# Performance work log

Measured on AMD Instinct MI355X. Metric: run time of the kernel, lower is better.

Reference implementation:

```python
import jax, jax.numpy as jnp
import numpy as np

HID = 1024   # hidden_size
NH = 16      # num_heads
NKV = 4      # num_kv_heads
HD = 64      # head_dim
C = 64       # chunk_size
RATIO = 0.125  # freq_cutoff_ratio
KS = 7       # conv_kernel_size


def setup_inputs() -> dict:
    key = jax.random.key(0)
    ks = jax.random.split(key, 11)
    B, N = 4, 4096
    s = 0.02
    return {
        "hidden_states": jax.random.normal(ks[0], (B, N, HID), jnp.float32),
        "q_w": jax.random.normal(ks[1], (NH * HD, HID), jnp.float32) * s,
        "k_w": jax.random.normal(ks[2], (NKV * HD, HID), jnp.float32) * s,
        "v_w": jax.random.normal(ks[3], (NKV * HD, HID), jnp.float32) * s,
        "o_w": jax.random.normal(ks[4], (HID, NH * HD), jnp.float32) * s,
        "dw_r": jax.random.normal(ks[5], (HID, 1, KS), jnp.float32) * 0.3,
        "pw_r": jax.random.normal(ks[6], (HID, HID), jnp.float32) * s,
        "dw_i": jax.random.normal(ks[7], (HID, 1, KS), jnp.float32) * 0.3,
        "pw_i": jax.random.normal(ks[8], (HID, HID), jnp.float32) * s,
        "gate_w": jax.random.normal(ks[9], (HID, HID), jnp.float32) * s,
        "alpha_raw": jnp.zeros((1,), jnp.float32),
    }


def _block_causal_attention(x, qw, kw, vw, ow, k):
    # x: [B, nc, k, D] real. Flatten chunk freq bins; chunk j attends to chunks 0..j.
    B, nc, _, D = x.shape
    T = nc * k
    xf = x.reshape(B, T, D)
    q = (xf @ qw.T).reshape(B, T, NH, HD).transpose(0, 2, 1, 3)    # [B,H,T,hd]
    kk = (xf @ kw.T).reshape(B, T, NKV, HD).transpose(0, 2, 1, 3)
    v = (xf @ vw.T).reshape(B, T, NKV, HD).transpose(0, 2, 1, 3)
    rep = NH // NKV
    kk = jnp.repeat(kk, rep, axis=1)
    v = jnp.repeat(v, rep, axis=1)
    chunk_ids = jnp.arange(T) // k
    mask = chunk_ids[:, None] >= chunk_ids[None, :]                # [T,T] bool
    scores = jnp.einsum('bhqd,bhkd->bhqk', q, kk) / np.float32(np.sqrt(HD))
    scores = jnp.where(mask[None, None], scores, jnp.finfo(scores.dtype).min)
    p = jax.nn.softmax(scores, axis=-1)
    o = jnp.einsum('bhqk,bhkd->bhqd', p, v)
    o = o.transpose(0, 2, 1, 3).reshape(B, T, NH * HD)
    return (o @ ow.T).reshape(B, nc, k, D)


def _causal_conv(x, dw, pw):
    # x: [B, nc, L, D] real. Depthwise causal conv + GELU + pointwise conv.
    B, nc, L, D = x.shape
    xc = x.reshape(B * nc, L, D).transpose(0, 2, 1)                # [BN, D, L]
    xp = jnp.pad(xc, ((0, 0), (0, 0), (KS - 1, 0)))                # causal left pad
    y = jax.lax.conv_general_dilated(
        xp, dw, window_strides=(1,), padding='VALID',
        dimension_numbers=('NCH', 'OIH', 'NCH'), feature_group_count=D)
    y = jax.nn.gelu(y, approximate=False)
    y = jnp.einsum('ncl,oc->nol', y, pw)                           # 1x1 conv
    return y.transpose(0, 2, 1).reshape(B, nc, L, D)


def _forward(hidden_states, q_w, k_w, v_w, o_w, dw_r, pw_r, dw_i, pw_i, gate_w, alpha_raw):
    B, N, D = hidden_states.shape
    pad_len = (-N) % C
    x = jnp.pad(hidden_states, ((0, 0), (0, pad_len), (0, 0))) if pad_len else hidden_states
    nc = x.shape[1] // C
    chunks = x.reshape(B, nc, C, D)
    Xh = jnp.fft.rfft(chunks.astype(jnp.float32), axis=2)          # [B,nc,M,D] complex
    M = Xh.shape[2]
    k = max(1, int(M * RATIO))
    X_low, X_high = Xh[:, :, :k, :], Xh[:, :, k:, :]
    # low-freq: block-causal attention on real and imag parts separately
    A_r = _block_causal_attention(X_low.real, q_w, k_w, v_w, o_w, k)
    A_i = _block_causal_attention(X_low.imag, q_w, k_w, v_w, o_w, k)
    A_low = jax.lax.complex(A_r, A_i)
    # high-freq: causal conv branch, gated by per-chunk time-domain mean
    H_r = _causal_conv(X_high.real, dw_r, pw_r)
    H_i = _causal_conv(X_high.imag, dw_i, pw_i)
    g = jax.nn.sigmoid(chunks.mean(axis=2) @ gate_w.T)[:, :, None, :]  # [B,nc,1,D]
    A_high = jax.lax.complex(H_r * g, H_i * g) + X_high
    alpha = jax.nn.sigmoid(alpha_raw)                               # [1]
    A_low_fused = alpha * A_low + (1.0 - alpha) * X_low
    Y_hat = jnp.concatenate([A_low_fused, A_high], axis=2)
    Y = jnp.fft.irfft(Y_hat, n=C, axis=2)
    return Y.reshape(B, -1, D)[:, :N, :].astype(hidden_states.dtype)


def reference(hidden_states, q_w, k_w, v_w, o_w, dw_r, pw_r, dw_i, pw_i, gate_w, alpha_raw):
    return _forward(hidden_states, q_w, k_w, v_w, o_w, dw_r, pw_r, dw_i, pw_i, gate_w, alpha_raw)
```

## Files before the change

### kernel.cpp

```cpp
#include <hip/hip_runtime.h>
#include <math.h>


typedef __bf16 bf16_t;
typedef bf16_t bf16x8 __attribute__((ext_vector_type(8)));
typedef float f32x4 __attribute__((ext_vector_type(4)));

#define EP_NONE 0
#define EP_SIGMOID 1
#define EP_FUSELOW 2
#define EP_HIGH 3

__device__ __forceinline__ void gld_lds16(const bf16_t* g, bf16_t* l) {
  __builtin_amdgcn_global_load_lds(
      (const __attribute__((address_space(1))) unsigned int*)g,
      (__attribute__((address_space(3))) unsigned int*)l, 16, 0, 0);
}

__global__ __launch_bounds__(256) void dft_kernel(const float* __restrict__ X,
                                                  bf16_t* __restrict__ Xh,
                                                  bf16_t* __restrict__ XLr,
                                                  bf16_t* __restrict__ XLi,
                                                  bf16_t* __restrict__ gmean) {
  const int d = blockIdx.x * 256 + threadIdx.x;
  const long bc = blockIdx.y;
  const int b = (int)(bc >> 6), ch = (int)(bc & 63);
  const float* xp = X + (bc * 64) * 1024 + d;
  float x[64];
#pragma unroll
  for (int t = 0; t < 64; t++) x[t] = xp[(long)t * 1024];
#pragma unroll
  for (int t = 0; t < 32; t++) {
    float a = x[t], bb = x[t + 32];
    x[t] = a + bb;
    x[t + 32] = a - bb;
  }
  bf16_t* outp = Xh + bc * 66 * 1024 + d;
  const float W = -6.283185307179586f / 64.f;
  for (int f = 0; f <= 32; f += 2) {
    float sd, cd;
    __sincosf(W * f, &sd, &cd);
    float c = 1.f, s = 0.f, ar = 0.f, ai = 0.f;
#pragma unroll
    for (int t = 0; t < 32; t++) {
      ar = fmaf(x[t], c, ar);
      ai = fmaf(x[t], s, ai);
      float cn = c * cd - s * sd;
      s = s * cd + c * sd;
      c = cn;
    }
    outp[(long)f * 1024] = (bf16_t)ar;
    outp[(long)(33 + f) * 1024] = (bf16_t)ai;
    if (f < 4) {
      long xr = ((long)(b * 256 + ch * 4 + f)) * 1024 + d;
      XLr[xr] = (bf16_t)ar;
      XLi[xr] = (bf16_t)ai;
    }
    if (f == 0) gmean[bc * 1024 + d] = (bf16_t)(ar * (1.f / 64.f));
  }
  for (int f = 1; f <= 31; f += 2) {
    float sd, cd;
    __sincosf(W * f, &sd, &cd);
    float c = 1.f, s = 0.f, ar = 0.f, ai = 0.f;
#pragma unroll
    for (int t = 0; t < 32; t++) {
      ar = fmaf(x[32 + t], c, ar);
      ai = fmaf(x[32 + t], s, ai);
      float cn = c * cd - s * sd;
      s = s * cd + c * sd;
      c = cn;
    }
    outp[(long)f * 1024] = (bf16_t)ar;
    outp[(long)(33 + f) * 1024] = (bf16_t)ai;
    if (f < 4) {
      long xr = ((long)(b * 256 + ch * 4 + f)) * 1024 + d;
      XLr[xr] = (bf16_t)ar;
      XLi[xr] = (bf16_t)ai;
    }
  }
}

__global__ __launch_bounds__(256) void concat_w(const float* __restrict__ qw,
                                                const float* __restrict__ kw,
                                                const float* __restrict__ vw,
                                                bf16_t* __restrict__ W) {
  int i = blockIdx.x * 256 + threadIdx.x;
  float4 v;
  if (i < 262144) v = ((const float4*)qw)[i];
  else if (i < 327680) v = ((const float4*)kw)[i - 262144];
  else v = ((const float4*)vw)[i - 327680];
  bf16_t* o = W + (long)i * 4;
  o[0] = (bf16_t)v.x; o[1] = (bf16_t)v.y; o[2] = (bf16_t)v.z; o[3] = (bf16_t)v.w;
}

__global__ __launch_bounds__(256) void cvt4_bf16(const float* __restrict__ s0,
                                                 const float* __restrict__ s1,
                                                 const float* __restrict__ s2,
                                                 const float* __restrict__ s3,
                                                 bf16_t* __restrict__ d0,
                                                 bf16_t* __restrict__ d1,
                                                 bf16_t* __restrict__ d2,
                                                 bf16_t* __restrict__ d3) {
  int i = blockIdx.x * 256 + threadIdx.x;
  const float* s = blockIdx.y == 0 ? s0 : blockIdx.y == 1 ? s1 : blockIdx.y == 2 ? s2 : s3;
  bf16_t* dst = blockIdx.y == 0 ? d0 : blockIdx.y == 1 ? d1 : blockIdx.y == 2 ? d2 : d3;
  float4 v = ((const float4*)s)[i];
  bf16_t* o = dst + (long)i * 4;
  o[0] = (bf16_t)v.x; o[1] = (bf16_t)v.y; o[2] = (bf16_t)v.z; o[3] = (bf16_t)v.w;
}

__global__ __launch_bounds__(256) void mk_basis(bf16_t* __restrict__ bhi,
                                                bf16_t* __restrict__ bres,
                                                float* __restrict__ tlow) {
  int idx = blockIdx.x * 256 + threadIdx.x;
  const float TW = 6.283185307179586f / 64.f;
  if (idx < 4096) {
    int t = idx >> 6, k = idx & 63;
    float v = 0.f;
    if (k < 28) {
      int ft = ((4 + k) * t) & 63;
      v = 2.f * cosf(TW * (float)ft) * (1.f / 64.f);
    } else if (k == 28) {
      int ft = (32 * t) & 63;
      v = cosf(TW * (float)ft) * (1.f / 64.f);
    } else if (k < 57) {
      int ft = ((k - 25) * t) & 63;
      v = -2.f * sinf(TW * (float)ft) * (1.f / 64.f);
    }
    bf16_t h = (bf16_t)v;
    float res = v - (float)h;
    int addr = t * 64 + (((k >> 3) ^ (t & 7)) << 3) + (k & 7);
    bhi[addr] = h;
    bres[addr] = (bf16_t)res;
  } else if (idx < 4608) {
    int i = idx - 4096;
    int t = i >> 3, j = i & 7;
    float v = 0.f;
    if (j == 0) v = 1.f / 64.f;
    else if (j < 7) {
      int f = (j + 1) >> 1;
      int ft = (f * t) & 63;
      float th = TW * (float)ft;
      v = (j & 1) ? 2.f * cosf(th) * (1.f / 64.f)
                  : -2.f * sinf(th) * (1.f / 64.f);
    }
    tlow[i] = v;
  }
}

template <int EMODE>
__global__ __launch_bounds__(256) void mmbf_kernel(
    const bf16_t* __restrict__ A0, const bf16_t* __restrict__ A1,
    const bf16_t* __restrict__ B0, const bf16_t* __restrict__ B1,
    int N, int K,
    void* __restrict__ C0v, void* __restrict__ C1v,
    const bf16_t* __restrict__ E0, const bf16_t* __restrict__ E1,
    bf16_t* __restrict__ XhMut,
    const float* __restrict__ gate, const float* __restrict__ alpha_ptr) {
  constexpr int BM = 128, BN = 128, BK = 32;
  __shared__ bf16_t As[BM * BK];
  __shared__ bf16_t Bs[BN * BK];
  const int z = blockIdx.z;
  const bf16_t* A = z ? A1 : A0;
  const bf16_t* B = z ? B1 : B0;
  void* Cv = z ? C1v : C0v;
  const bf16_t* E = z ? E1 : E0;
  const int imoff = z ? 33 * 1024 : 0;
  const int tid = threadIdx.x;
  const int lane = tid & 63;
  const int wave = tid >> 6;
  const int wm = (wave & 1) * 64, wn = (wave >> 1) * 64;
  const int m0 = blockIdx.x * BM, n0 = blockIdx.y * BN;
  const int q = lane >> 4, mr = lane & 15;
  const int lrow = lane >> 2, lk8 = (lane & 3) * 8;

  f32x4 acc[4][4];
#pragma unroll
  for (int i = 0; i < 4; i++)
#pragma unroll
    for (int j = 0; j < 4; j++) acc[i][j] = (f32x4){0.f, 0.f, 0.f, 0.f};

  const long arow0 = (long)(m0 + wave * 16 + lrow) * K + lk8;
  const long brow0 = (long)(n0 + wave * 16 + lrow) * K + lk8;

  for (int kb = 0; kb < K; kb += BK) {
#pragma unroll
    for (int it = 0; it < 2; it++) {
      gld_lds16(A + arow0 + (long)it * 64 * K + kb, As + (wave * 16 + it * 64) * BK);
      gld_lds16(B + brow0 + (long)it * 64 * K + kb, Bs + (wave * 16 + it * 64) * BK);
    }
    __syncthreads();
    bf16x8 af[4], bfr[4];
#pragma unroll
    for (int mi = 0; mi < 4; mi++)
      af[mi] = *(const bf16x8*)&As[(wm + mi * 16 + mr) * BK + q * 8];
#pragma unroll
    for (int ni = 0; ni < 4; ni++)
      bfr[ni] = *(const bf16x8*)&Bs[(wn + ni * 16 + mr) * BK + q * 8];
#pragma unroll
    for (int mi = 0; mi < 4; mi++)
#pragma unroll
      for (int ni = 0; ni < 4; ni++)
        acc[mi][ni] = __builtin_amdgcn_mfma_f32_16x16x32_bf16(
            af[mi], bfr[ni], acc[mi][ni], 0, 0, 0);
    __syncthreads();
  }

  float alpha = 0.f;
  if constexpr (EMODE == EP_FUSELOW) alpha = 1.f / (1.f + __expf(-alpha_ptr[0]));
#pragma unroll
  for (int mi = 0; mi < 4; mi++) {
#pragma unroll
    for (int ni = 0; ni < 4; ni++) {
      int col = n0 + wn + ni * 16 + mr;
      int rbase = m0 + wm + mi * 16 + q * 4;
#pragma unroll
      for (int r = 0; r < 4; r++) {
        int row = rbase + r;
        float val = acc[mi][ni][r];
        if constexpr (EMODE == EP_NONE) {
          ((bf16_t*)Cv)[(long)row * N + col] = (bf16_t)val;
        } else if constexpr (EMODE == EP_SIGMOID) {
          ((float*)Cv)[(long)row * N + col] = 1.f / (1.f + __expf(-val));
        } else if constexpr (EMODE == EP_FUSELOW) {
          float xl = (float)E[(long)row * 1024 + col];
          ((float*)Cv)[(long)row * 1024 + col] = alpha * val + (1.f - alpha) * xl;
        } else {
          int bc = row / 29, l = row - bc * 29;
          long x = ((long)bc * 66 + 4 + l) * 1024 + imoff + col;
          XhMut[x] = (bf16_t)fmaf(val, gate[(long)bc * 1024 + col], (float)XhMut[x]);
        }
      }
    }
  }
}

__global__ __launch_bounds__(512, 2) void gemm256_high(
    const bf16_t* __restrict__ A0, const bf16_t* __restrict__ A1,
    const bf16_t* __restrict__ B0, const bf16_t* __restrict__ B1,
    bf16_t* __restrict__ XhMut, const float* __restrict__ gate) {
  constexpr int K = 1024;
  constexpr int NT = K / 32;
  __shared__ bf16_t lds[4][2][256 * 32];

  const int id = blockIdx.x;
  const int kk = (id & 7) * 29 + (id >> 3);
  const int mt = kk >> 3, rem = kk & 7;
  const int nt = rem & 3, z = rem >> 2;
  const bf16_t* A = z ? A1 : A0;
  const bf16_t* B = z ? B1 : B0;
  const int imoff = z ? 33 * 1024 : 0;
  const int m0 = mt * 256, n0 = nt * 256;

  const int tid = threadIdx.x;
  const int lane = tid & 63, wave = tid >> 6;
  const int wm = (wave & 1) * 128, wn = (wave >> 1) * 64;
  const int q = lane >> 4, mr = lane & 15;
  const int srow = tid >> 2;
  const int gk8 = (((tid & 3) ^ ((tid >> 2) & 3)) << 3);

  f32x4 acc[8][4];
#pragma unroll
  for (int i = 0; i < 8; i++)
#pragma unroll
    for (int j = 0; j < 4; j++) acc[i][j] = (f32x4){0.f, 0.f, 0.f, 0.f};

  auto stage = [&](int t) {
    const int bi = t & 3;
    const int kb = t * 32;
#pragma unroll
    for (int rd = 0; rd < 2; rd++) {
      gld_lds16(A + (long)(m0 + rd * 128 + srow) * K + kb + gk8,
                &lds[bi][0][(rd * 512 + wave * 64) * 8]);
      gld_lds16(B + (long)(n0 + rd * 128 + srow) * K + kb + gk8,
                &lds[bi][1][(rd * 512 + wave * 64) * 8]);
    }
  };

  stage(0);
  stage(1);
  stage(2);

  const int asl = (q ^ (mr & 3)) * 8;

  for (int t = 0; t < NT; t++) {
    if (t < NT - 2)
      asm volatile("s_waitcnt vmcnt(8)" ::: "memory");
    else if (t == NT - 2)
      asm volatile("s_waitcnt vmcnt(4)" ::: "memory");
    else
      asm volatile("s_waitcnt vmcnt(0)" ::: "memory");
    __builtin_amdgcn_sched_barrier(0);
    __builtin_amdgcn_s_barrier();
    if (t + 3 < NT) stage(t + 3);

    const bf16_t* As_ = &lds[t & 3][0][0];
    const bf16_t* Bs_ = &lds[t & 3][1][0];
    bf16x8 bfr[4];
#pragma unroll
    for (int ni = 0; ni < 4; ni++)
      bfr[ni] = *(const bf16x8*)&Bs_[(wn + ni * 16 + mr) * 32 + asl];
    __builtin_amdgcn_s_setprio(1);
#pragma unroll
    for (int mi = 0; mi < 8; mi++) {
      bf16x8 af = *(const bf16x8*)&As_[(wm + mi * 16 + mr) * 32 + asl];
#pragma unroll
      for (int ni = 0; ni < 4; ni++)
        acc[mi][ni] = __builtin_amdgcn_mfma_f32_16x16x32_bf16(
            af, bfr[ni], acc[mi][ni], 0, 0, 0);
    }
    __builtin_amdgcn_s_setprio(0);
  }

#pragma unroll
  for (int mi = 0; mi < 8; mi++) {
#pragma unroll
    for (int r = 0; r < 4; r++) {
      int row = m0 + wm + mi * 16 + q * 4 + r;
      int bc = row / 29, l = row - bc * 29;
      long xbase = ((long)bc * 66 + 4 + l) * 1024 + imoff;
      const float* gp = gate + (long)bc * 1024;
#pragma unroll
      for (int ni = 0; ni < 4; ni++) {
        int col = n0 + wn + ni * 16 + mr;
        long x = xbase + col;
        XhMut[x] = (bf16_t)fmaf(acc[mi][ni][r], gp[col], (float)XhMut[x]);
      }
    }
  }
}

__global__ __launch_bounds__(256) void attn_mfma(const bf16_t* __restrict__ QKVr,
                                                 const bf16_t* __restrict__ QKVi,
                                                 bf16_t* __restrict__ Or_,
                                                 bf16_t* __restrict__ Oi_) {
  const int h = blockIdx.x;
  const int b = blockIdx.y >> 2, qt = blockIdx.y & 3;
  const bf16_t* QKV = blockIdx.z ? QKVi : QKVr;
  bf16_t* O = blockIdx.z ? Oi_ : Or_;
  const int kvh = h >> 2;
  const int tid = threadIdx.x;
  const int lane = tid & 63, wave = tid >> 6;
  const int mr = lane & 15, q4 = lane >> 4;

  __shared__ bf16_t Ks[64 * 72];
  __shared__ bf16_t Vt[64 * 72];
  __shared__ bf16_t Ps[4][16 * 72];

  bf16x8 af[2];
  {
    const bf16_t* qp =
        QKV + (long)(b * 256 + qt * 64 + wave * 16 + mr) * 1536 + h * 64;
    af[0] = *(const bf16x8*)(qp + q4 * 8);
    af[1] = *(const bf16x8*)(qp + 32 + q4 * 8);
  }
  f32x4 Oacc[4];
#pragma unroll
  for (int ni = 0; ni < 4; ni++) Oacc[ni] = (f32x4){0.f, 0.f, 0.f, 0.f};
  float mrow[4], lrow[4];
#pragma unroll
  for (int r = 0; r < 4; r++) { mrow[r] = -1e30f; lrow[r] = 0.f; }

  for (int kt = 0; kt <= qt; kt++) {
#pragma unroll
    for (int it = 0; it < 2; it++) {
      int idx = tid + it * 256;
      int key = idx >> 3, dg = idx & 7;
      const bf16_t* kp = QKV + (long)(b * 256 + kt * 64 + key) * 1536 + 1024 +
                         kvh * 64 + dg * 8;
      *(bf16x8*)&Ks[key * 72 + dg * 8] = *(const bf16x8*)kp;
      bf16x8 vv = *(const bf16x8*)(kp + 256);
#pragma unroll
      for (int j = 0; j < 8; j++) Vt[(dg * 8 + j) * 72 + key] = vv[j];
    }
    __syncthreads();

    f32x4 S[4];
#pragma unroll
    for (int ni = 0; ni < 4; ni++) {
      S[ni] = (f32x4){0.f, 0.f, 0.f, 0.f};
#pragma unroll
      for (int s = 0; s < 2; s++) {
        bf16x8 kb = *(const bf16x8*)&Ks[(ni * 16 + mr) * 72 + s * 32 + q4 * 8];
        S[ni] = __builtin_amdgcn_mfma_f32_16x16x32_bf16(af[s], kb, S[ni], 0, 0, 0);
      }
    }
#pragma unroll
    for (int ni = 0; ni < 4; ni++) {
#pragma unroll
      for (int r = 0; r < 4; r++) {
        float v = S[ni][r] * 0.125f;
        if (kt == qt) {
          int qrow = wave * 16 + q4 * 4 + r;
          int kcol = ni * 16 + mr;
          if ((qrow >> 2) < (kcol >> 2)) v = -1e30f;
        }
        S[ni][r] = v;
      }
    }
#pragma unroll
    for (int r = 0; r < 4; r++) {
      float mx = fmaxf(fmaxf(S[0][r], S[1][r]), fmaxf(S[2][r], S[3][r]));
#pragma unroll
      for (int off = 1; off < 16; off <<= 1) mx = fmaxf(mx, __shfl_xor(mx, off));
      float mn = fmaxf(mrow[r], mx);
      float sc = __expf(mrow[r] - mn);
      mrow[r] = mn;
      float rs = 0.f;
#pragma unroll
      for (int ni = 0; ni < 4; ni++) {
        float p = __expf(S[ni][r] - mn);
        rs += p;
        Ps[wave][(q4 * 4 + r) * 72 + ni * 16 + mr] = (bf16_t)p;
      }
#pragma unroll
      for (int off = 1; off < 16; off <<= 1) rs += __shfl_xor(rs, off);
      lrow[r] = lrow[r] * sc + rs;
#pragma unroll
      for (int ni = 0; ni < 4; ni++) Oacc[ni][r] *= sc;
    }
    bf16x8 pa[2];
    pa[0] = *(const bf16x8*)&Ps[wave][mr * 72 + q4 * 8];
    pa[1] = *(const bf16x8*)&Ps[wave][mr * 72 + 32 + q4 * 8];
#pragma unroll
    for (int ni = 0; ni < 4; ni++) {
#pragma unroll
      for (int s = 0; s < 2; s++) {
        bf16x8 vb = *(const bf16x8*)&Vt[(ni * 16 + mr) * 72 + s * 32 + q4 * 8];
        Oacc[ni] = __builtin_amdgcn_mfma_f32_16x16x32_bf16(pa[s], vb, Oacc[ni], 0, 0, 0);
      }
    }
    __syncthreads();
  }

#pragma unroll
  for (int r = 0; r < 4; r++) {
    float inv = 1.f / lrow[r];
    long row = b * 256 + qt * 64 + wave * 16 + q4 * 4 + r;
#pragma unroll
    for (int ni = 0; ni < 4; ni++)
      O[row * 1024 + h * 64 + ni * 16 + mr] = (bf16_t)(Oacc[ni][r] * inv);
  }
}

__global__ __launch_bounds__(256) void dwconv_kernel(const bf16_t* __restrict__ Xh,
                                                     const float* __restrict__ dwr,
                                                     const float* __restrict__ dwi,
                                                     bf16_t* __restrict__ Gr,
                                                     bf16_t* __restrict__ Gi) {
  const int d = blockIdx.x * 256 + threadIdx.x;
  const int bc = blockIdx.y;
  const float* dw = blockIdx.z ? dwi : dwr;
  bf16_t* G = blockIdx.z ? Gi : Gr;
  const int imoff = blockIdx.z ? 33 * 1024 : 0;
  float w[7];
#pragma unroll
  for (int j = 0; j < 7; j++) w[j] = dw[d * 7 + j];
  float x[29];
#pragma unroll
  for (int l = 0; l < 29; l++)
    x[l] = (float)Xh[((long)bc * 66 + 4 + l) * 1024 + imoff + d];
#pragma unroll
  for (int l = 0; l < 29; l++) {
    float y = 0.f;
#pragma unroll
    for (int j = 0; j < 7; j++) {
      int src = l - 6 + j;
      if (src >= 0) y = fmaf(w[j], x[src], y);
    }
    float ge = 0.5f * y * (1.f + erff(y * 0.7071067811865475f));
    G[((long)bc * 29 + l) * 1024 + d] = (bf16_t)ge;
  }
}

__global__ __launch_bounds__(256) void irfft_mfma(
    const bf16_t* __restrict__ Xh, const float* __restrict__ Afr,
    const float* __restrict__ Afi, const bf16_t* __restrict__ bhi,
    const bf16_t* __restrict__ bres, const float* __restrict__ tlow,
    float* __restrict__ out) {
  const int bc = blockIdx.y;
  const int d0 = blockIdx.x * 256;
  const int tid = threadIdx.x;
  const int lane = tid & 63, wave = tid >> 6;
  const int mr = lane & 15, q = lane >> 4;
  const int wn = wave * 64;

  __shared__ bf16_t Ahi[64 * 64];
  __shared__ bf16_t Ares[64 * 64];
  __shared__ bf16_t Bs[256 * 64];
  __shared__ float Tl[64 * 8];

  gld_lds16(bhi + (wave * 64 + lane) * 8, Ahi + wave * 64 * 8);
  gld_lds16(bhi + (256 + wave * 64 + lane) * 8, Ahi + (256 + wave * 64) * 8);
  gld_lds16(bres + (wave * 64 + lane) * 8, Ares + wave * 64 * 8);
  gld_lds16(bres + (256 + wave * 64 + lane) * 8, Ares + (256 + wave * 64) * 8);
  if (tid < 128) ((float4*)Tl)[tid] = ((const float4*)tlow)[tid];

  {
    const bf16_t* xc = Xh + (long)bc * 66 * 1024 + d0 + tid;
    const int sw = tid & 7;
#pragma unroll
    for (int g = 0; g < 8; g++) {
      bf16x8 v;
#pragma unroll
      for (int i = 0; i < 8; i++) {
        int j = g * 8 + i;
        int row = (j < 29) ? (4 + j) : (8 + j);
        v[i] = (j < 57) ? xc[(long)row * 1024] : (bf16_t)0.f;
      }
      *(bf16x8*)&Bs[tid * 64 + ((g ^ sw) << 3)] = v;
    }
  }
  __syncthreads();

  f32x4 acc[4][4];
#pragma unroll
  for (int i = 0; i < 4; i++)
#pragma unroll
    for (int j = 0; j < 4; j++) acc[i][j] = (f32x4){0.f, 0.f, 0.f, 0.f};

#pragma unroll
  for (int s = 0; s < 2; s++) {
    bf16x8 bfv[4];
#pragma unroll
    for (int ni = 0; ni < 4; ni++) {
      int dcol = wn + ni * 16 + mr;
      bfv[ni] = *(const bf16x8*)&Bs[dcol * 64 + (((s * 4 + q) ^ (dcol & 7)) << 3)];
    }
#pragma unroll
    for (int mi = 0; mi < 4; mi++) {
      int trow = mi * 16 + mr;
      int so = (((s * 4 + q) ^ (trow & 7)) << 3);
      bf16x8 ah = *(const bf16x8*)&Ahi[trow * 64 + so];
      bf16x8 ar = *(const bf16x8*)&Ares[trow * 64 + so];
#pragma unroll
      for (int ni = 0; ni < 4; ni++) {
        acc[mi][ni] = __builtin_amdgcn_mfma_f32_16x16x32_bf16(
            ah, bfv[ni], acc[mi][ni], 0, 0, 0);
        acc[mi][ni] = __builtin_amdgcn_mfma_f32_16x16x32_bf16(
            ar, bfv[ni], acc[mi][ni], 0, 0, 0);
      }
    }
  }

  const int arow = (bc >> 6) * 256 + (bc & 63) * 4;
  float R[4][7];
#pragma unroll
  for (int ni = 0; ni < 4; ni++) {
    long ab = (long)arow * 1024 + d0 + wn + ni * 16 + mr;
    R[ni][0] = Afr[ab];
    R[ni][1] = Afr[ab + 1024];
    R[ni][2] = Afi[ab + 1024];
    R[ni][3] = Afr[ab + 2048];
    R[ni][4] = Afi[ab + 2048];
    R[ni][5] = Afr[ab + 3072];
    R[ni][6] = Afi[ab + 3072];
  }
  const long obase = ((long)bc * 64) * 1024 + d0;
#pragma unroll
  for (int mi = 0; mi < 4; mi++) {
#pragma unroll
    for (int r = 0; r < 4; r++) {
      int t = mi * 16 + q * 4 + r;
      const float* tl = &Tl[t * 8];
#pragma unroll
      for (int ni = 0; ni < 4; ni++) {
        float low = tl[0] * R[ni][0];
        low = fmaf(tl[1], R[ni][1], low);
        low = fmaf(tl[2], R[ni][2], low);
        low = fmaf(tl[3], R[ni][3], low);
        low = fmaf(tl[4], R[ni][4], low);
        low = fmaf(tl[5], R[ni][5], low);
        low = fmaf(tl[6], R[ni][6], low);
        out[obase + (long)t * 1024 + wn + ni * 16 + mr] = acc[mi][ni][r] + low;
      }
    }
  }
}

extern "C" void kernel_launch(void* const* d_in, const int* in_sizes, int n_in,
                              void* d_out, int out_size, void* d_ws, size_t ws_size,
                              hipStream_t stream) {
  const float* hidden = (const float*)d_in[0];
  const float* q_w = (const float*)d_in[1];
  const float* k_w = (const float*)d_in[2];
  const float* v_w = (const float*)d_in[3];
  const float* o_w = (const float*)d_in[4];
  const float* dw_r = (const float*)d_in[5];
  const float* pw_r = (const float*)d_in[6];
  const float* dw_i = (const float*)d_in[7];
  const float* pw_i = (const float*)d_in[8];
  const float* gate_w = (const float*)d_in[9];
  const float* alpha_raw = (const float*)d_in[10];
  float* out = (float*)d_out;

  float* ws = (float*)d_ws;
  float* Afr = ws;
  float* Afi = Afr + 1048576;
  float* gg = Afi + 1048576;
  bf16_t* bws = (bf16_t*)(gg + 262144);
  bf16_t* Xh = bws;
  bf16_t* Wqkv_b = Xh + 17301504;
  bf16_t* ow_b = Wqkv_b + 1572864;
  bf16_t* gw_b = ow_b + 1048576;
  bf16_t* pwr_b = gw_b + 1048576;
  bf16_t* pwi_b = pwr_b + 1048576;
  bf16_t* XLr = pwi_b + 1048576;
  bf16_t* XLi = XLr + 1048576;
  bf16_t* gmean = XLi + 1048576;
  bf16_t* QKVbr = gmean + 262144;
  bf16_t* QKVbi = QKVbr + 1572864;
  bf16_t* Obr = QKVbi + 1572864;
  bf16_t* Obi = Obr + 1048576;
  bf16_t* Gr = Obi + 1048576;
  bf16_t* Gi = Gr + 7602176;
  bf16_t* bhi = Gi + 7602176;
  bf16_t* bres = bhi + 4096;
  float* tlowp = (float*)(bres + 4096);

  mk_basis<<<18, 256, 0, stream>>>(bhi, bres, tlowp);
  dft_kernel<<<dim3(4, 256), 256, 0, stream>>>(hidden, Xh, XLr, XLi, gmean);
  concat_w<<<1536, 256, 0, stream>>>(q_w, k_w, v_w, Wqkv_b);
  cvt4_bf16<<<dim3(1024, 4), 256, 0, stream>>>(o_w, gate_w, pw_r, pw_i,
                                               ow_b, gw_b, pwr_b, pwi_b);
  mmbf_kernel<EP_NONE><<<dim3(8, 12, 2), 256, 0, stream>>>(
      XLr, XLi, Wqkv_b, Wqkv_b, 1536, 1024, QKVbr, QKVbi, nullptr, nullptr,
      nullptr, nullptr, nullptr);
  mmbf_kernel<EP_SIGMOID><<<dim3(2, 8, 1), 256, 0, stream>>>(
      gmean, gmean, gw_b, gw_b, 1024, 1024, gg, gg, nullptr, nullptr,
      nullptr, nullptr, nullptr);
  attn_mfma<<<dim3(16, 16, 2), 256, 0, stream>>>(QKVbr, QKVbi, Obr, Obi);
  mmbf_kernel<EP_FUSELOW><<<dim3(8, 8, 2), 256, 0, stream>>>(
      Obr, Obi, ow_b, ow_b, 1024, 1024, Afr, Afi, XLr, XLi,
      nullptr, nullptr, alpha_raw);
  dwconv_kernel<<<dim3(4, 256, 2), 256, 0, stream>>>(Xh, dw_r, dw_i, Gr, Gi);
  gemm256_high<<<dim3(232), 512, 0, stream>>>(Gr, Gi, pwr_b, pwi_b, Xh, gg);
  irfft_mfma<<<dim3(4, 256), 256, 0, stream>>>(Xh, Afr, Afi, bhi, bres,
                                               tlowp, out);
}
```

Baseline: 347.9 us.

## Compute forward chunk DFT with split-bf16 MFMA against precomputed basis

Replaces the scalar per-thread DFT kernel with an MFMA-based kernel that multiplies a precomputed cos/sin basis (split into bf16 hi and residual parts) against the input chunk, also split into hi and residual parts staged in swizzled LDS. Three MFMA products recover near-fp32 accuracy, moving the DFT onto the matrix cores instead of long serial FMA/rotation chains. The basis generation kernel is extended to also emit the DFT basis. Separately, the LDS swizzle in the 256-tile GEMM is changed to reduce bank conflicts. The DFT gains extra LDS traffic and a residual-split precision approximation.

Result: no change. 343.6 us (-1.2%).

```diff
diff --git a/kernel.cpp b/kernel.cpp
--- a/kernel.cpp
+++ b/kernel.cpp
@@ -15,69 +15,6 @@
   __builtin_amdgcn_global_load_lds(
       (const __attribute__((address_space(1))) unsigned int*)g,
       (__attribute__((address_space(3))) unsigned int*)l, 16, 0, 0);
-}
-
-__global__ __launch_bounds__(256) void dft_kernel(const float* __restrict__ X,
-                                                  bf16_t* __restrict__ Xh,
-                                                  bf16_t* __restrict__ XLr,
-                                                  bf16_t* __restrict__ XLi,
-                                                  bf16_t* __restrict__ gmean) {
-  const int d = blockIdx.x * 256 + threadIdx.x;
-  const long bc = blockIdx.y;
-  const int b = (int)(bc >> 6), ch = (int)(bc & 63);
-  const float* xp = X + (bc * 64) * 1024 + d;
-  float x[64];
-#pragma unroll
-  for (int t = 0; t < 64; t++) x[t] = xp[(long)t * 1024];
-#pragma unroll
-  for (int t = 0; t < 32; t++) {
-    float a = x[t], bb = x[t + 32];
-    x[t] = a + bb;
-    x[t + 32] = a - bb;
-  }
-  bf16_t* outp = Xh + bc * 66 * 1024 + d;
-  const float W = -6.283185307179586f / 64.f;
-  for (int f = 0; f <= 32; f += 2) {
-    float sd, cd;
-    __sincosf(W * f, &sd, &cd);
-    float c = 1.f, s = 0.f, ar = 0.f, ai = 0.f;
-#pragma unroll
-    for (int t = 0; t < 32; t++) {
-      ar = fmaf(x[t], c, ar);
-      ai = fmaf(x[t], s, ai);
-      float cn = c * cd - s * sd;
-      s = s * cd + c * sd;
-      c = cn;
-    }
-    outp[(long)f * 1024] = (bf16_t)ar;
-    outp[(long)(33 + f) * 1024] = (bf16_t)ai;
-    if (f < 4) {
-      long xr = ((long)(b * 256 + ch * 4 + f)) * 1024 + d;
-      XLr[xr] = (bf16_t)ar;
-      XLi[xr] = (bf16_t)ai;
-    }
-    if (f == 0) gmean[bc * 1024 + d] = (bf16_t)(ar * (1.f / 64.f));
-  }
-  for (int f = 1; f <= 31; f += 2) {
-    float sd, cd;
-    __sincosf(W * f, &sd, &cd);
-    float c = 1.f, s = 0.f, ar = 0.f, ai = 0.f;
-#pragma unroll
-    for (int t = 0; t < 32; t++) {
-      ar = fmaf(x[32 + t], c, ar);
-      ai = fmaf(x[32 + t], s, ai);
-      float cn = c * cd - s * sd;
-      s = s * cd + c * sd;
-      c = cn;
-    }
-    outp[(long)f * 1024] = (bf16_t)ar;
-    outp[(long)(33 + f) * 1024] = (bf16_t)ai;
-    if (f < 4) {
-      long xr = ((long)(b * 256 + ch * 4 + f)) * 1024 + d;
-      XLr[xr] = (bf16_t)ar;
-      XLi[xr] = (bf16_t)ai;
-    }
-  }
 }
 
 __global__ __launch_bounds__(256) void concat_w(const float* __restrict__ qw,
@@ -109,13 +46,29 @@
   o[0] = (bf16_t)v.x; o[1] = (bf16_t)v.y; o[2] = (bf16_t)v.z; o[3] = (bf16_t)v.w;
 }
 
-__global__ __launch_bounds__(256) void mk_basis(bf16_t* __restrict__ bhi,
+__global__ __launch_bounds__(256) void mk_basis(bf16_t* __restrict__ dhi,
+                                                bf16_t* __restrict__ dres,
+                                                bf16_t* __restrict__ bhi,
                                                 bf16_t* __restrict__ bres,
                                                 float* __restrict__ tlow) {
   int idx = blockIdx.x * 256 + threadIdx.x;
   const float TW = 6.283185307179586f / 64.f;
-  if (idx < 4096) {
-    int t = idx >> 6, k = idx & 63;
+  if (idx < 5120) {
+    int r = idx >> 6, k = idx & 63;
+    float v = 0.f;
+    if (r < 33) {
+      v = cosf(TW * (float)((r * k) & 63));
+    } else if (r < 66) {
+      v = -sinf(TW * (float)(((r - 33) * k) & 63));
+    }
+    bf16_t h = (bf16_t)v;
+    float res = v - (float)h;
+    int addr = r * 64 + (((k >> 3) ^ (r & 7)) << 3) + (k & 7);
+    dhi[addr] = h;
+    dres[addr] = (bf16_t)res;
+  } else if (idx < 9216) {
+    int i = idx - 5120;
+    int t = i >> 6, k = i & 63;
     float v = 0.f;
     if (k < 28) {
       int ft = ((4 + k) * t) & 63;
@@ -132,8 +85,8 @@
     int addr = t * 64 + (((k >> 3) ^ (t & 7)) << 3) + (k & 7);
     bhi[addr] = h;
     bres[addr] = (bf16_t)res;
-  } else if (idx < 4608) {
-    int i = idx - 4096;
+  } else if (idx < 9728) {
+    int i = idx - 9216;
     int t = i >> 3, j = i & 7;
     float v = 0.f;
     if (j == 0) v = 1.f / 64.f;
@@ -145,6 +98,106 @@
                   : -2.f * sinf(th) * (1.f / 64.f);
     }
     tlow[i] = v;
+  }
+}
+
+__global__ __launch_bounds__(256) void dft_mfma(
+    const float* __restrict__ X, const bf16_t* __restrict__ dhi,
+    const bf16_t* __restrict__ dres, bf16_t* __restrict__ Xh,
+    bf16_t* __restrict__ XLr, bf16_t* __restrict__ XLi,
+    bf16_t* __restrict__ gmean) {
+  const int bc = blockIdx.y;
+  const int d0 = blockIdx.x * 256;
+  const int tid = threadIdx.x;
+  const int lane = tid & 63, wave = tid >> 6;
+  const int mr = lane & 15, q = lane >> 4;
+  const int wn = wave * 64;
+
+  __shared__ bf16_t Ahi[80 * 64];
+  __shared__ bf16_t Ares[80 * 64];
+  __shared__ bf16_t Bh[256 * 64];
+  __shared__ bf16_t Br[256 * 64];
+
+  for (int i = wave; i < 10; i += 4) {
+    gld_lds16(dhi + (i * 64 + lane) * 8, Ahi + i * 512);
+    gld_lds16(dres + (i * 64 + lane) * 8, Ares + i * 512);
+  }
+
+  {
+    const float* xc = X + ((long)bc * 64) * 1024 + d0 + tid;
+    const int sw = tid & 7;
+#pragma unroll
+    for (int g = 0; g < 8; g++) {
+      bf16x8 vh, vr;
+#pragma unroll
+      for (int i = 0; i < 8; i++) {
+        float v = xc[(long)(g * 8 + i) * 1024];
+        bf16_t h = (bf16_t)v;
+        vh[i] = h;
+        vr[i] = (bf16_t)(v - (float)h);
+      }
+      *(bf16x8*)&Bh[tid * 64 + ((g ^ sw) << 3)] = vh;
+      *(bf16x8*)&Br[tid * 64 + ((g ^ sw) << 3)] = vr;
+    }
+  }
+  __syncthreads();
+
+  f32x4 acc[5][4];
+#pragma unroll
+  for (int i = 0; i < 5; i++)
+#pragma unroll
+    for (int j = 0; j < 4; j++) acc[i][j] = (f32x4){0.f, 0.f, 0.f, 0.f};
+
+#pragma unroll
+  for (int s = 0; s < 2; s++) {
+    bf16x8 bh[4], br[4];
+#pragma unroll
+    for (int ni = 0; ni < 4; ni++) {
+      int dcol = wn + ni * 16 + mr;
+      int so = (((s * 4 + q) ^ (dcol & 7)) << 3);
+      bh[ni] = *(const bf16x8*)&Bh[dcol * 64 + so];
+      br[ni] = *(const bf16x8*)&Br[dcol * 64 + so];
+    }
+#pragma unroll
+    for (int mi = 0; mi < 5; mi++) {
+      int trow = mi * 16 + mr;
+      int so = (((s * 4 + q) ^ (trow & 7)) << 3);
+      bf16x8 ah = *(const bf16x8*)&Ahi[trow * 64 + so];
+      bf16x8 ar = *(const bf16x8*)&Ares[trow * 64 + so];
+#pragma unroll
+      for (int ni = 0; ni < 4; ni++) {
+        acc[mi][ni] = __builtin_amdgcn_mfma_f32_16x16x32_bf16(
+            ah, bh[ni], acc[mi][ni], 0, 0, 0);
+        acc[mi][ni] = __builtin_amdgcn_mfma_f32_16x16x32_bf16(
+            ah, br[ni], acc[mi][ni], 0, 0, 0);
+        acc[mi][ni] = __builtin_amdgcn_mfma_f32_16x16x32_bf16(
+            ar, bh[ni], acc[mi][ni], 0, 0, 0);
+      }
+    }
+  }
+
+  const int b = bc >> 6, ch = bc & 63;
+  bf16_t* xp = Xh + (long)bc * 66 * 1024 + d0;
+#pragma unroll
+  for (int mi = 0; mi < 5; mi++) {
+#pragma unroll
+    for (int r = 0; r < 4; r++) {
+      int row = mi * 16 + q * 4 + r;
+      if (row >= 66) continue;
+#pragma unroll
+      for (int ni = 0; ni < 4; ni++) {
+        int col = wn + ni * 16 + mr;
+        float val = acc[mi][ni][r];
+        xp[(long)row * 1024 + col] = (bf16_t)val;
+        if (row == 0)
+          gmean[(long)bc * 1024 + d0 + col] = (bf16_t)(val * (1.f / 64.f));
+        if (row < 4)
+          XLr[((long)(b * 256 + ch * 4 + row)) * 1024 + d0 + col] = (bf16_t)val;
+        if (row >= 33 && row < 37)
+          XLi[((long)(b * 256 + ch * 4 + row - 33)) * 1024 + d0 + col] =
+              (bf16_t)val;
+      }
+    }
   }
 }
 
@@ -257,7 +310,7 @@
   const int wm = (wave & 1) * 128, wn = (wave >> 1) * 64;
   const int q = lane >> 4, mr = lane & 15;
   const int srow = tid >> 2;
-  const int gk8 = (((tid & 3) ^ ((tid >> 2) & 3)) << 3);
+  const int gk8 = (((tid & 3) ^ ((((tid >> 2) & 3) + ((tid >> 4) & 3)) & 3)) << 3);
 
   f32x4 acc[8][4];
 #pragma unroll
@@ -281,7 +334,7 @@
   stage(1);
   stage(2);
 
-  const int asl = (q ^ (mr & 3)) * 8;
+  const int asl = (q ^ (((mr & 3) + ((mr >> 2) & 3)) & 3)) * 8;
 
   for (int t = 0; t < NT; t++) {
     if (t < NT - 2)
@@ -616,10 +669,13 @@
   bf16_t* Gi = Gr + 7602176;
   bf16_t* bhi = Gi + 7602176;
   bf16_t* bres = bhi + 4096;
-  float* tlowp = (float*)(bres + 4096);
-
-  mk_basis<<<18, 256, 0, stream>>>(bhi, bres, tlowp);
-  dft_kernel<<<dim3(4, 256), 256, 0, stream>>>(hidden, Xh, XLr, XLi, gmean);
+  bf16_t* dbhi = bres + 4096;
+  bf16_t* dbres = dbhi + 5120;
+  float* tlowp = (float*)(dbres + 5120);
+
+  mk_basis<<<38, 256, 0, stream>>>(dbhi, dbres, bhi, bres, tlowp);
+  dft_mfma<<<dim3(4, 256), 256, 0, stream>>>(hidden, dbhi, dbres, Xh, XLr,
+                                             XLi, gmean);
   concat_w<<<1536, 256, 0, stream>>>(q_w, k_w, v_w, Wqkv_b);
   cvt4_bf16<<<dim3(1024, 4), 256, 0, stream>>>(o_w, gate_w, pw_r, pw_i,
                                                ow_b, gw_b, pwr_b, pwi_b);
```
